# Kernel optimization log

Hardware: AMD Instinct MI355X
Metric: run time of the kernel (lower is better)

The kernel has to match this reference:

```python
import jax, jax.numpy as jnp
import numpy as np

N, E, B, DIM, NF, EF, HID = 16384, 32768, 512, 64, 14, 4, 128

def _p(key, shape, scale):
    return jax.random.normal(key, shape, dtype=jnp.float32) * scale

def setup_inputs() -> dict:
    key = jax.random.key(0)
    ks = jax.random.split(key, 20)
    s = lambda fan: 1.0 / float(np.sqrt(fan))
    z = lambda *sh: jnp.zeros(sh, jnp.float32)
    return {
        "x": jax.random.normal(ks[0], (N, NF), dtype=jnp.float32),
        "edge_index": jax.random.randint(ks[1], (2, E), 0, N),
        "edge_attr": jax.random.uniform(ks[2], (E, EF), dtype=jnp.float32),
        "batch": jnp.sort(jax.random.randint(ks[3], (N,), 0, B)),
        "do_dropout": 0,
        "mlp_drop": 0,
        "lin0_w": _p(ks[4], (NF, DIM), s(NF)), "lin0_b": z(DIM),
        "nn1_w": _p(ks[5], (EF, HID), s(EF)), "nn1_b": z(HID),
        "nn2_w": _p(ks[6], (HID, DIM * DIM), s(HID)), "nn2_b": z(DIM * DIM),
        "root_w": _p(ks[7], (DIM, DIM), s(DIM)), "conv_b": z(DIM),
        "gru_w_ih": _p(ks[8], (3 * DIM, DIM), s(DIM)), "gru_w_hh": _p(ks[9], (3 * DIM, DIM), s(DIM)),
        "gru_b_ih": _p(ks[10], (3 * DIM,), s(DIM)), "gru_b_hh": _p(ks[11], (3 * DIM,), s(DIM)),
        "lstm_w_ih": _p(ks[12], (4 * DIM, 2 * DIM), s(DIM)), "lstm_w_hh": _p(ks[13], (4 * DIM, DIM), s(DIM)),
        "lstm_b_ih": _p(ks[14], (4 * DIM,), s(DIM)), "lstm_b_hh": _p(ks[15], (4 * DIM,), s(DIM)),
        "lin1_w": _p(ks[16], (2 * DIM, DIM), s(2 * DIM)), "lin1_b": z(DIM),
        "lin2_w": _p(ks[17], (DIM, 1), s(DIM)), "lin2_b": z(1),
    }

def _forward(x, edge_attr, lin0_w, lin0_b, nn1_w, nn1_b, nn2_w, nn2_b, root_w, conv_b,
             gru_w_ih, gru_w_hh, gru_b_ih, gru_b_hh,
             lstm_w_ih, lstm_w_hh, lstm_b_ih, lstm_b_hh,
             lin1_w, lin1_b, lin2_w, lin2_b, edge_index, batch):
    src, dst = edge_index[0], edge_index[1]
    out = jax.nn.relu(x @ lin0_w + lin0_b)                      # [N, DIM]
    h = out
    # Edge-conditioned weights (edge_attr is layer-independent -> compute once)
    ew = jax.nn.relu(edge_attr @ nn1_w + nn1_b) @ nn2_w + nn2_b  # [E, DIM*DIM]
    ew = ew.reshape(E, DIM, DIM)
    deg = jax.ops.segment_sum(jnp.ones((E,), jnp.float32), dst, num_segments=N)
    deg = jnp.maximum(deg, 1.0)[:, None]                        # mean aggregation denominator

    def gru_cell(xin, hprev):
        gi = xin @ gru_w_ih.T + gru_b_ih
        gh = hprev @ gru_w_hh.T + gru_b_hh
        ir, iz, inn = jnp.split(gi, 3, axis=-1)
        hr, hz, hn = jnp.split(gh, 3, axis=-1)
        r = jax.nn.sigmoid(ir + hr)
        zg = jax.nn.sigmoid(iz + hz)
        n = jnp.tanh(inn + r * hn)
        return (1.0 - zg) * n + zg * hprev

    for _ in range(3):  # 3 message-passing rounds (structurally fixed)
        msg = jnp.einsum('ed,edf->ef', out[src], ew)            # gather -> per-edge matvec
        agg = jax.ops.segment_sum(msg, dst, num_segments=N) / deg
        m = jax.nn.relu(out @ root_w + agg + conv_b)            # NNConv (root weight + mean aggr)
        h = gru_cell(m, h)
        out = h

    # Set2Set pooling, 3 processing steps
    q_star = jnp.zeros((B, 2 * DIM), jnp.float32)
    hl = jnp.zeros((B, DIM), jnp.float32)
    cl = jnp.zeros((B, DIM), jnp.float32)
    for _ in range(3):
        gates = q_star @ lstm_w_ih.T + lstm_b_ih + hl @ lstm_w_hh.T + lstm_b_hh
        ii, ff, gg, oo = jnp.split(gates, 4, axis=-1)
        cl = jax.nn.sigmoid(ff) * cl + jax.nn.sigmoid(ii) * jnp.tanh(gg)
        hl = jax.nn.sigmoid(oo) * jnp.tanh(cl)
        q = hl                                                  # [B, DIM]
        e = jnp.sum(out * q[batch], axis=-1)                    # [N]
        emax = jax.ops.segment_max(e, batch, num_segments=B)
        ex = jnp.exp(e - emax[batch])
        esum = jnp.maximum(jax.ops.segment_sum(ex, batch, num_segments=B), 1e-16)
        a = ex / esum[batch]                                    # segment softmax
        r = jax.ops.segment_sum(a[:, None] * out, batch, num_segments=B)
        q_star = jnp.concatenate([q, r], axis=-1)               # [B, 2*DIM]

    y = jax.nn.relu(q_star @ lin1_w + lin1_b)
    # dropout flags are False (eval) -> identity
    y = y @ lin2_w + lin2_b
    return y.reshape(-1)                                        # [B]

def reference(x, edge_index, edge_attr, batch, do_dropout, mlp_drop,
              lin0_w, lin0_b, nn1_w, nn1_b, nn2_w, nn2_b, root_w, conv_b,
              gru_w_ih, gru_w_hh, gru_b_ih, gru_b_hh,
              lstm_w_ih, lstm_w_hh, lstm_b_ih, lstm_b_hh,
              lin1_w, lin1_b, lin2_w, lin2_b):
    return _forward(x, edge_attr, lin0_w, lin0_b, nn1_w, nn1_b, nn2_w, nn2_b, root_w, conv_b,
                    gru_w_ih, gru_w_hh, gru_b_ih, gru_b_hh,
                    lstm_w_ih, lstm_w_hh, lstm_b_ih, lstm_b_hh,
                    lin1_w, lin1_b, lin2_w, lin2_b, edge_index, batch)
```

## Files before the change

kernel.cpp:

```cpp
#include <hip/hip_runtime.h>
#include <math.h>

#define N_NODES 16384
#define N_EDGES 32768
#define NGRAPH  512
#define DIM     64
#define NF      14
#define HIDN    128
#define EWCOLS  4096

typedef unsigned short u16;
typedef unsigned int   u32;
typedef __attribute__((ext_vector_type(8))) short bf16x8;
typedef __attribute__((ext_vector_type(4))) float f32x4;
typedef __attribute__((ext_vector_type(4))) u32   u32x4;

__device__ inline float b2f(u16 u){
    unsigned int x = ((unsigned int)u) << 16;
    return __builtin_bit_cast(float, x);
}
__device__ inline u16 f2b(float f){
    unsigned int x = __builtin_bit_cast(unsigned int, f);
    unsigned int r = (x + 0x7FFFu + ((x >> 16) & 1u)) >> 16;
    return (u16)r;
}
__device__ inline float sigf(float x){ return 1.f / (1.f + expf(-x)); }

__global__ __launch_bounds__(256) void k_lin0(const float* __restrict__ x,
        const float* __restrict__ w, const float* __restrict__ b, float* __restrict__ out){
    int n = (blockIdx.x * blockDim.x + threadIdx.x) >> 6;
    int lane = threadIdx.x & 63;
    if (n >= N_NODES) return;
    float xv = (lane < NF) ? x[n * NF + lane] : 0.f;
    float acc = b[lane];
    #pragma unroll
    for (int d = 0; d < NF; ++d){
        float xd = __shfl(xv, d);
        acc += xd * w[d * DIM + lane];
    }
    out[n * DIM + lane] = fmaxf(acc, 0.f);
}

__global__ __launch_bounds__(256) void k_prep(const float* __restrict__ w2,
        const float* __restrict__ lwih, const float* __restrict__ lwhh,
        const float* __restrict__ root, const float* __restrict__ gwih, const float* __restrict__ gwhh,
        u16* __restrict__ w2T, float* __restrict__ wihT, float* __restrict__ whhT,
        u16* __restrict__ rtHi, u16* __restrict__ rtLo,
        u16* __restrict__ wihHi, u16* __restrict__ wihLo,
        u16* __restrict__ whhHi, u16* __restrict__ whhLo){
    int i = blockIdx.x * 256 + threadIdx.x;
    if (i < 524288){
        int k = i >> 12, c = i & 4095;
        w2T[c * HIDN + k] = f2b(w2[i]);
    } else if (i < 557056){
        int i2 = i - 524288;
        int j = i2 >> 7, d = i2 & 127;
        wihT[d * 256 + j] = lwih[i2];
    } else if (i < 573440){
        int i2 = i - 557056;
        int j = i2 >> 6, d = i2 & 63;
        whhT[d * 256 + j] = lwhh[i2];
    } else if (i < 577536){
        int i2 = i - 573440;
        int d = i2 >> 6, j = i2 & 63;
        float v = root[i2]; u16 h = f2b(v);
        rtHi[j * 64 + d] = h; rtLo[j * 64 + d] = f2b(v - b2f(h));
    } else if (i < 589824){
        int k = i - 577536;
        float v = gwih[k]; u16 h = f2b(v);
        wihHi[k] = h; wihLo[k] = f2b(v - b2f(h));
    } else if (i < 602112){
        int k = i - 589824;
        float v = gwhh[k]; u16 h = f2b(v);
        whhHi[k] = h; whhLo[k] = f2b(v - b2f(h));
    }
}

__global__ __launch_bounds__(256) void k_deg(const int* __restrict__ ei, unsigned* __restrict__ degu){
    int e = blockIdx.x * blockDim.x + threadIdx.x;
    if (e < N_EDGES) atomicAdd(&degu[ei[N_EDGES + e]], 1u);
}
__global__ __launch_bounds__(256) void k_dinv(const unsigned* __restrict__ degu, float* __restrict__ dinv){
    int n = blockIdx.x * blockDim.x + threadIdx.x;
    if (n < N_NODES) dinv[n] = 1.f / fmaxf((float)degu[n], 1.f);
}

#define EB   64
#define LDO  68

__global__ __launch_bounds__(256) void k_msg_fused(
        const int* __restrict__ ei, const float* __restrict__ ea,
        const float* __restrict__ w1, const float* __restrict__ b1,
        const u16* __restrict__ w2T, const float* __restrict__ b2,
        const float* __restrict__ out, float* __restrict__ agg)
{
    __shared__ float s_out[EB * LDO];
    __shared__ u16   s_b[2][64 * 128];
    __shared__ float s_w1[512];
    __shared__ float s_b1[128];
    int tid = threadIdx.x;
    int e0 = blockIdx.x * EB;

    s_w1[tid] = w1[tid];
    s_w1[tid + 256] = w1[tid + 256];
    if (tid < 128) s_b1[tid] = b1[tid];
    {
        int row = tid >> 2, cb = (tid & 3) * 16;
        int s = ei[e0 + row];
        const float4* sp = (const float4*)(out + (size_t)s * DIM + cb);
        float4 v0 = sp[0], v1 = sp[1], v2 = sp[2], v3 = sp[3];
        float* dst = s_out + row * LDO + cb;
        *(float4*)(dst)      = v0;
        *(float4*)(dst + 4)  = v1;
        *(float4*)(dst + 8)  = v2;
        *(float4*)(dst + 12) = v3;
    }
    __syncthreads();

    int wv = tid >> 6, lane = tid & 63;
    int WR = (wv >> 1) * 32, WC = (wv & 1) * 32;
    int lr = lane & 15, lk = (lane >> 4) * 8;

    bf16x8 afr[2][4];
    #pragma unroll
    for (int m = 0; m < 2; ++m){
        int erow = e0 + WR + m*16 + lr;
        float4 av = *(const float4*)(ea + (size_t)erow * 4);
        #pragma unroll
        for (int kk = 0; kk < 4; ++kk){
            bf16x8 t8;
            #pragma unroll
            for (int i = 0; i < 8; ++i){
                int h = kk*32 + lk + i;
                float acc = s_b1[h] + av.x*s_w1[h] + av.y*s_w1[128+h]
                          + av.z*s_w1[256+h] + av.w*s_w1[384+h];
                t8[i] = (short)f2b(fmaxf(acc, 0.f));
            }
            afr[m][kk] = t8;
        }
    }

    int bc = tid >> 2, bs = tid & 3;
    const u32x4* gb = (const u32x4*)w2T;
    u32x4 rg[4];
    #pragma unroll
    for (int q = 0; q < 4; ++q) rg[q] = gb[((size_t)bc << 4) + bs*4 + q];

    f32x4 msg[2][2] = {};
    int swzr = (lr & 7) << 4;
    int swzw = (bc & 7) << 4;
    int crow = (lane >> 4) * 4;

    for (int d = 0; d < 64; ++d){
        char* sw = (char*)s_b[d & 1];
        #pragma unroll
        for (int q = 0; q < 4; ++q)
            *(u32x4*)(sw + ((bc*256 + (bs*4+q)*16) ^ swzw)) = rg[q];
        if (d < 63){
            #pragma unroll
            for (int q = 0; q < 4; ++q)
                rg[q] = gb[(((size_t)(d+1)*64 + bc) << 4) + bs*4 + q];
        }
        __syncthreads();
        const char* sr = (const char*)s_b[d & 1];
        f32x4 ew[2][2] = {};
        #pragma unroll
        for (int kk = 0; kk < 4; ++kk){
            int kb = kk*64 + (lane >> 4) * 16;
            bf16x8 bf0 = *(const bf16x8*)(sr + (((WC + lr)*256 + kb)      ^ swzr));
            bf16x8 bf1 = *(const bf16x8*)(sr + (((WC + 16 + lr)*256 + kb) ^ swzr));
            ew[0][0] = __builtin_amdgcn_mfma_f32_16x16x32_bf16(afr[0][kk], bf0, ew[0][0], 0, 0, 0);
            ew[0][1] = __builtin_amdgcn_mfma_f32_16x16x32_bf16(afr[0][kk], bf1, ew[0][1], 0, 0, 0);
            ew[1][0] = __builtin_amdgcn_mfma_f32_16x16x32_bf16(afr[1][kk], bf0, ew[1][0], 0, 0, 0);
            ew[1][1] = __builtin_amdgcn_mfma_f32_16x16x32_bf16(afr[1][kk], bf1, ew[1][1], 0, 0, 0);
        }
        int f0 = d*64 + WC + lr;
        float b2v0 = b2[f0], b2v1 = b2[f0 + 16];
        #pragma unroll
        for (int m = 0; m < 2; ++m){
            #pragma unroll
            for (int r = 0; r < 4; ++r){
                float sc = s_out[(WR + m*16 + crow + r) * LDO + d];
                msg[m][0][r] += sc * (ew[m][0][r] + b2v0);
                msg[m][1][r] += sc * (ew[m][1][r] + b2v1);
            }
        }
    }

    #pragma unroll
    for (int m = 0; m < 2; ++m){
        #pragma unroll
        for (int r = 0; r < 4; ++r){
            int eg = e0 + WR + m*16 + crow + r;
            int dn = ei[N_EDGES + eg];
            atomicAdd(&agg[(size_t)dn * DIM + WC + lr],      msg[m][0][r]);
            atomicAdd(&agg[(size_t)dn * DIM + WC + 16 + lr], msg[m][1][r]);
        }
    }
}

#define LDH 68
__global__ __launch_bounds__(256) void k_update(
        const u16* __restrict__ rtHi, const u16* __restrict__ rtLo,
        const u16* __restrict__ wihHi, const u16* __restrict__ wihLo,
        const u16* __restrict__ whhHi, const u16* __restrict__ whhLo,
        const float* __restrict__ convb, const float* __restrict__ bih,
        const float* __restrict__ bhh,
        const float* __restrict__ agg, const float* __restrict__ dinv,
        float* __restrict__ out)
{
    __shared__ float s_h[64 * LDH];
    __shared__ float s_aux[64 * LDH];
    __shared__ float s_m[64 * LDH];
    int tid = threadIdx.x;
    int n0 = blockIdx.x * 64;

    {
        int row = tid >> 2, cb = (tid & 3) * 16;
        const float4* hp = (const float4*)(out + (size_t)(n0 + row) * DIM + cb);
        const float4* ap = (const float4*)(agg + (size_t)(n0 + row) * DIM + cb);
        float di = dinv[n0 + row];
        #pragma unroll
        for (int q = 0; q < 4; ++q){
            float4 hv = hp[q];
            float4 av = ap[q];
            *(float4*)(s_h + row * LDH + cb + q*4) = hv;
            float4 xv;
            xv.x = av.x * di + convb[cb + q*4 + 0];
            xv.y = av.y * di + convb[cb + q*4 + 1];
            xv.z = av.z * di + convb[cb + q*4 + 2];
            xv.w = av.w * di + convb[cb + q*4 + 3];
            *(float4*)(s_aux + row * LDH + cb + q*4) = xv;
        }
    }
    __syncthreads();

    int wv = tid >> 6, lane = tid & 63;
    int lr = lane & 15, lkb = (lane >> 4) * 8;
    int arow = wv * 16 + lr;

    bf16x8 hHi[2], hLo[2];
    #pragma unroll
    for (int kk = 0; kk < 2; ++kk){
        const float* src = s_h + arow * LDH + kk*32 + lkb;
        bf16x8 hi8, lo8;
        #pragma unroll
        for (int e = 0; e < 8; ++e){
            float v = src[e];
            u16 h = f2b(v);
            hi8[e] = (short)h;
            lo8[e] = (short)f2b(v - b2f(h));
        }
        hHi[kk] = hi8; hLo[kk] = lo8;
    }

    f32x4 c1[4] = {};
    #pragma unroll
    for (int ct = 0; ct < 4; ++ct){
        #pragma unroll
        for (int kk = 0; kk < 2; ++kk){
            int off = (ct*16 + lr) * 64 + kk*32 + lkb;
            bf16x8 bHi = *(const bf16x8*)(rtHi + off);
            bf16x8 bLo = *(const bf16x8*)(rtLo + off);
            c1[ct] = __builtin_amdgcn_mfma_f32_16x16x32_bf16(hHi[kk], bHi, c1[ct], 0, 0, 0);
            c1[ct] = __builtin_amdgcn_mfma_f32_16x16x32_bf16(hLo[kk], bHi, c1[ct], 0, 0, 0);
            c1[ct] = __builtin_amdgcn_mfma_f32_16x16x32_bf16(hHi[kk], bLo, c1[ct], 0, 0, 0);
        }
    }

    int crow = (lane >> 4) * 4;
    #pragma unroll
    for (int ct = 0; ct < 4; ++ct){
        #pragma unroll
        for (int r = 0; r < 4; ++r){
            int row = wv*16 + crow + r;
            int col = ct*16 + lr;
            float m = fmaxf(c1[ct][r] + s_aux[row * LDH + col], 0.f);
            s_m[row * LDH + col] = m;
        }
    }
    __syncthreads();

    bf16x8 mHi[2], mLo[2];
    #pragma unroll
    for (int kk = 0; kk < 2; ++kk){
        const float* src = s_m + arow * LDH + kk*32 + lkb;
        bf16x8 hi8, lo8;
        #pragma unroll
        for (int e = 0; e < 8; ++e){
            float v = src[e];
            u16 h = f2b(v);
            hi8[e] = (short)h;
            lo8[e] = (short)f2b(v - b2f(h));
        }
        mHi[kk] = hi8; mLo[kk] = lo8;
    }

    f32x4 gi[12] = {}, gh[12] = {};
    #pragma unroll
    for (int ct = 0; ct < 12; ++ct){
        #pragma unroll
        for (int kk = 0; kk < 2; ++kk){
            int off = (ct*16 + lr) * 64 + kk*32 + lkb;
            bf16x8 biH = *(const bf16x8*)(wihHi + off);
            bf16x8 biL = *(const bf16x8*)(wihLo + off);
            gi[ct] = __builtin_amdgcn_mfma_f32_16x16x32_bf16(mHi[kk], biH, gi[ct], 0, 0, 0);
            gi[ct] = __builtin_amdgcn_mfma_f32_16x16x32_bf16(mLo[kk], biH, gi[ct], 0, 0, 0);
            gi[ct] = __builtin_amdgcn_mfma_f32_16x16x32_bf16(mHi[kk], biL, gi[ct], 0, 0, 0);
            bf16x8 bhH = *(const bf16x8*)(whhHi + off);
            bf16x8 bhL = *(const bf16x8*)(whhLo + off);
            gh[ct] = __builtin_amdgcn_mfma_f32_16x16x32_bf16(hHi[kk], bhH, gh[ct], 0, 0, 0);
            gh[ct] = __builtin_amdgcn_mfma_f32_16x16x32_bf16(hLo[kk], bhH, gh[ct], 0, 0, 0);
            gh[ct] = __builtin_amdgcn_mfma_f32_16x16x32_bf16(hHi[kk], bhL, gh[ct], 0, 0, 0);
        }
    }

    #pragma unroll
    for (int ct = 0; ct < 4; ++ct){
        int col = ct*16 + lr;
        float br_i = bih[col],       br_h = bhh[col];
        float bz_i = bih[64 + col],  bz_h = bhh[64 + col];
        float bn_i = bih[128 + col], bn_h = bhh[128 + col];
        #pragma unroll
        for (int r = 0; r < 4; ++r){
            int row = wv*16 + crow + r;
            float rg = sigf(gi[ct][r] + br_i + gh[ct][r] + br_h);
            float zg = sigf(gi[ct+4][r] + bz_i + gh[ct+4][r] + bz_h);
            float ng = tanhf(gi[ct+8][r] + bn_i + rg * (gh[ct+8][r] + bn_h));
            float h  = s_h[row * LDH + col];
            s_aux[row * LDH + col] = (1.f - zg) * ng + zg * h;
        }
    }
    __syncthreads();

    {
        int row = tid >> 2, cb = (tid & 3) * 16;
        #pragma unroll
        for (int q = 0; q < 4; ++q)
            *(float4*)(out + (size_t)(n0 + row) * DIM + cb + q*4) =
                *(const float4*)(s_aux + row * LDH + cb + q*4);
    }
}

__global__ __launch_bounds__(256) void k_s2s(
        const float* __restrict__ out, const int* __restrict__ batch,
        const float* __restrict__ wihT, const float* __restrict__ lbih,
        const float* __restrict__ whhT, const float* __restrict__ lbhh,
        const float* __restrict__ l1w, const float* __restrict__ l1b,
        const float* __restrict__ l2w, const float* __restrict__ l2b,
        float* __restrict__ ebuf, float* __restrict__ y)
{
    __shared__ float s_q[128];
    __shared__ float s_hc[128];
    __shared__ float s_g[256];
    __shared__ float s_rw[256];
    __shared__ float s_sw[8];
    __shared__ int   s_rng[2];
    int g = blockIdx.x, tid = threadIdx.x;
    if (tid < 2){
        int target = g + tid;
        int lo = 0, hi = N_NODES;
        while (lo < hi){ int mid = (lo + hi) >> 1; if (batch[mid] < target) lo = mid + 1; else hi = mid; }
        s_rng[tid] = lo;
    }
    if (tid < 128){ s_q[tid] = 0.f; s_hc[tid] = 0.f; }
    __syncthreads();
    int s0 = s_rng[0], s1 = s_rng[1];
    int wv = tid >> 6, lane = tid & 63;

    for (int step = 0; step < 3; ++step){
        float acc = lbih[tid] + lbhh[tid];
        #pragma unroll 8
        for (int d = 0; d < 128; ++d) acc += s_q[d] * wihT[d * 256 + tid];
        #pragma unroll 8
        for (int d = 0; d < 64;  ++d) acc += s_hc[d] * whhT[d * 256 + tid];
        s_g[tid] = acc;
        __syncthreads();
        if (tid < 64){
            float c = sigf(s_g[64 + tid]) * s_hc[64 + tid] + sigf(s_g[tid]) * tanhf(s_g[128 + tid]);
            float h = sigf(s_g[192 + tid]) * tanhf(c);
            s_hc[tid] = h; s_hc[64 + tid] = c;
            s_q[tid] = h;
        }
        __syncthreads();
        float q = s_hc[lane];
        float emx = -3.4e38f;
        for (int n = s0 + wv; n < s1; n += 4){
            float v = out[(size_t)n * DIM + lane] * q;
            #pragma unroll
            for (int off = 32; off; off >>= 1) v += __shfl_xor(v, off);
            if (lane == 0) ebuf[n] = v;
            emx = fmaxf(emx, v);
        }
        if (lane == 0) s_sw[wv] = emx;
        __syncthreads();
        float gmax = fmaxf(fmaxf(s_sw[0], s_sw[1]), fmaxf(s_sw[2], s_sw[3]));
        float rl = 0.f, ss = 0.f;
        for (int n = s0 + wv; n < s1; n += 4){
            float ex = expf(ebuf[n] - gmax);
            rl += ex * out[(size_t)n * DIM + lane];
            ss += ex;
        }
        s_rw[wv * 64 + lane] = rl;
        if (lane == 0) s_sw[4 + wv] = ss;
        __syncthreads();
        if (tid < 64){
            float r = s_rw[tid] + s_rw[64 + tid] + s_rw[128 + tid] + s_rw[192 + tid];
            float S = fmaxf(s_sw[4] + s_sw[5] + s_sw[6] + s_sw[7], 1e-16f);
            s_q[64 + tid] = r / S;
        }
        __syncthreads();
    }
    if (wv == 0){
        float acc = l1b[lane];
        #pragma unroll 8
        for (int d = 0; d < 128; ++d) acc += s_q[d] * l1w[d * 64 + lane];
        float h = fmaxf(acc, 0.f);
        float p = h * l2w[lane];
        #pragma unroll
        for (int off = 32; off; off >>= 1) p += __shfl_down(p, off);
        if (lane == 0) y[g] = p + l2b[0];
    }
}

extern "C" void kernel_launch(void* const* d_in, const int* in_sizes, int n_in,
                              void* d_out, int out_size, void* d_ws, size_t ws_size,
                              hipStream_t stream){
    const float* x      = (const float*)d_in[0];
    const int*   ei     = (const int*)d_in[1];
    const float* ea     = (const float*)d_in[2];
    const int*   batch  = (const int*)d_in[3];
    const float* lin0_w = (const float*)d_in[6];
    const float* lin0_b = (const float*)d_in[7];
    const float* nn1_w  = (const float*)d_in[8];
    const float* nn1_b  = (const float*)d_in[9];
    const float* nn2_w  = (const float*)d_in[10];
    const float* nn2_b  = (const float*)d_in[11];
    const float* root_w = (const float*)d_in[12];
    const float* conv_b = (const float*)d_in[13];
    const float* gwih   = (const float*)d_in[14];
    const float* gwhh   = (const float*)d_in[15];
    const float* gbih   = (const float*)d_in[16];
    const float* gbhh   = (const float*)d_in[17];
    const float* lwih   = (const float*)d_in[18];
    const float* lwhh   = (const float*)d_in[19];
    const float* lbih   = (const float*)d_in[20];
    const float* lbhh   = (const float*)d_in[21];
    const float* l1w    = (const float*)d_in[22];
    const float* l1b    = (const float*)d_in[23];
    const float* l2w    = (const float*)d_in[24];
    const float* l2b    = (const float*)d_in[25];
    float* y = (float*)d_out;

    char* p = (char*)d_ws;
    float* out   = (float*)p;    p += (size_t)N_NODES * DIM * 4;
    float* agg   = (float*)p;    p += (size_t)N_NODES * DIM * 4;
    u16* w2T     = (u16*)p;      p += (size_t)EWCOLS * HIDN * 2;
    float* wihT  = (float*)p;    p += 128 * 256 * 4;
    float* whhT  = (float*)p;    p += 64 * 256 * 4;
    u16* rtHi    = (u16*)p;      p += 4096 * 2;
    u16* rtLo    = (u16*)p;      p += 4096 * 2;
    u16* wihHi   = (u16*)p;      p += 12288 * 2;
    u16* wihLo   = (u16*)p;      p += 12288 * 2;
    u16* whhHi   = (u16*)p;      p += 12288 * 2;
    u16* whhLo   = (u16*)p;      p += 12288 * 2;
    unsigned* degu = (unsigned*)p; p += N_NODES * 4;
    float* dinv  = (float*)p;    p += N_NODES * 4;
    float* ebuf  = (float*)p;    p += N_NODES * 4;

    if ((size_t)(p - (char*)d_ws) > ws_size) return;

    hipMemsetAsync(degu, 0, N_NODES * 4, stream);

    k_prep<<<2352, 256, 0, stream>>>(nn2_w, lwih, lwhh, root_w, gwih, gwhh,
                w2T, wihT, whhT, rtHi, rtLo, wihHi, wihLo, whhHi, whhLo);
    k_lin0<<<N_NODES / 4, 256, 0, stream>>>(x, lin0_w, lin0_b, out);
    k_deg <<<N_EDGES / 256, 256, 0, stream>>>(ei, degu);
    k_dinv<<<N_NODES / 256, 256, 0, stream>>>(degu, dinv);

    for (int r = 0; r < 3; ++r){
        hipMemsetAsync(agg, 0, (size_t)N_NODES * DIM * 4, stream);
        k_msg_fused<<<N_EDGES / EB, 256, 0, stream>>>(ei, ea, nn1_w, nn1_b, w2T, nn2_b, out, agg);
        k_update   <<<N_NODES / 64, 256, 0, stream>>>(rtHi, rtLo, wihHi, wihLo, whhHi, whhLo,
                        conv_b, gbih, gbhh, agg, dinv, out);
    }

    k_s2s<<<NGRAPH, 256, 0, stream>>>(out, batch, wihT, lbih, whhT, lbhh,
                l1w, l1b, l2w, l2b, ebuf, y);
}
```

Before: 370.0 us.

## Double edge tile per message block to halve nn2 weight streaming; stage bias in LDS

```diff
diff --git a/kernel.cpp b/kernel.cpp
--- a/kernel.cpp
+++ b/kernel.cpp
@@ -85,10 +85,10 @@
     if (n < N_NODES) dinv[n] = 1.f / fmaxf((float)degu[n], 1.f);
 }
 
-#define EB   64
+#define EB   128
 #define LDO  68
 
-__global__ __launch_bounds__(256) void k_msg_fused(
+__global__ __launch_bounds__(512) void k_msg_fused(
         const int* __restrict__ ei, const float* __restrict__ ea,
         const float* __restrict__ w1, const float* __restrict__ b1,
         const u16* __restrict__ w2T, const float* __restrict__ b2,
@@ -96,14 +96,19 @@
 {
     __shared__ float s_out[EB * LDO];
     __shared__ u16   s_b[2][64 * 128];
+    __shared__ float s_b2[EWCOLS];
     __shared__ float s_w1[512];
     __shared__ float s_b1[128];
     int tid = threadIdx.x;
     int e0 = blockIdx.x * EB;
 
     s_w1[tid] = w1[tid];
-    s_w1[tid + 256] = w1[tid + 256];
     if (tid < 128) s_b1[tid] = b1[tid];
+    {
+        int base = tid * 8;
+        *(float4*)(s_b2 + base)     = *(const float4*)(b2 + base);
+        *(float4*)(s_b2 + base + 4) = *(const float4*)(b2 + base + 4);
+    }
     {
         int row = tid >> 2, cb = (tid & 3) * 16;
         int s = ei[e0 + row];
@@ -140,11 +145,10 @@
         }
     }
 
-    int bc = tid >> 2, bs = tid & 3;
+    int bc = tid >> 3, bs = tid & 7;
     const u32x4* gb = (const u32x4*)w2T;
-    u32x4 rg[4];
-    #pragma unroll
-    for (int q = 0; q < 4; ++q) rg[q] = gb[((size_t)bc << 4) + bs*4 + q];
+    u32x4 r0 = gb[((size_t)bc << 4) + bs*2];
+    u32x4 r1 = gb[((size_t)bc << 4) + bs*2 + 1];
 
     f32x4 msg[2][2] = {};
     int swzr = (lr & 7) << 4;
@@ -153,13 +157,12 @@
 
     for (int d = 0; d < 64; ++d){
         char* sw = (char*)s_b[d & 1];
-        #pragma unroll
-        for (int q = 0; q < 4; ++q)
-            *(u32x4*)(sw + ((bc*256 + (bs*4+q)*16) ^ swzw)) = rg[q];
+        *(u32x4*)(sw + ((bc*256 + bs*32)      ^ swzw)) = r0;
+        *(u32x4*)(sw + ((bc*256 + bs*32 + 16) ^ swzw)) = r1;
         if (d < 63){
-            #pragma unroll
-            for (int q = 0; q < 4; ++q)
-                rg[q] = gb[(((size_t)(d+1)*64 + bc) << 4) + bs*4 + q];
+            size_t base = ((size_t)(d+1)*64 + bc) << 4;
+            r0 = gb[base + bs*2];
+            r1 = gb[base + bs*2 + 1];
         }
         __syncthreads();
         const char* sr = (const char*)s_b[d & 1];
@@ -174,8 +177,8 @@
             ew[1][0] = __builtin_amdgcn_mfma_f32_16x16x32_bf16(afr[1][kk], bf0, ew[1][0], 0, 0, 0);
             ew[1][1] = __builtin_amdgcn_mfma_f32_16x16x32_bf16(afr[1][kk], bf1, ew[1][1], 0, 0, 0);
         }
-        int f0 = d*64 + WC + lr;
-        float b2v0 = b2[f0], b2v1 = b2[f0 + 16];
+        float b2v0 = s_b2[d*64 + WC + lr];
+        float b2v1 = s_b2[d*64 + WC + 16 + lr];
         #pragma unroll
         for (int m = 0; m < 2; ++m){
             #pragma unroll
@@ -348,7 +351,7 @@
         const float* __restrict__ whhT, const float* __restrict__ lbhh,
         const float* __restrict__ l1w, const float* __restrict__ l1b,
         const float* __restrict__ l2w, const float* __restrict__ l2b,
-        float* __restrict__ ebuf, float* __restrict__ y)
+        float* __restrict__ y)
 {
     __shared__ float s_q[128];
     __shared__ float s_hc[128];
@@ -389,7 +392,6 @@
             float v = out[(size_t)n * DIM + lane] * q;
             #pragma unroll
             for (int off = 32; off; off >>= 1) v += __shfl_xor(v, off);
-            if (lane == 0) ebuf[n] = v;
             emx = fmaxf(emx, v);
         }
         if (lane == 0) s_sw[wv] = emx;
@@ -397,8 +399,12 @@
         float gmax = fmaxf(fmaxf(s_sw[0], s_sw[1]), fmaxf(s_sw[2], s_sw[3]));
         float rl = 0.f, ss = 0.f;
         for (int n = s0 + wv; n < s1; n += 4){
-            float ex = expf(ebuf[n] - gmax);
-            rl += ex * out[(size_t)n * DIM + lane];
+            float o = out[(size_t)n * DIM + lane];
+            float v = o * q;
+            #pragma unroll
+            for (int off = 32; off; off >>= 1) v += __shfl_xor(v, off);
+            float ex = expf(v - gmax);
+            rl += ex * o;
             ss += ex;
         }
         s_rw[wv * 64 + lane] = rl;
@@ -466,7 +472,6 @@
     u16* whhLo   = (u16*)p;      p += 12288 * 2;
     unsigned* degu = (unsigned*)p; p += N_NODES * 4;
     float* dinv  = (float*)p;    p += N_NODES * 4;
-    float* ebuf  = (float*)p;    p += N_NODES * 4;
 
     if ((size_t)(p - (char*)d_ws) > ws_size) return;
 
@@ -480,11 +485,11 @@
 
     for (int r = 0; r < 3; ++r){
         hipMemsetAsync(agg, 0, (size_t)N_NODES * DIM * 4, stream);
-        k_msg_fused<<<N_EDGES / EB, 256, 0, stream>>>(ei, ea, nn1_w, nn1_b, w2T, nn2_b, out, agg);
+        k_msg_fused<<<N_EDGES / EB, 512, 0, stream>>>(ei, ea, nn1_w, nn1_b, w2T, nn2_b, out, agg);
         k_update   <<<N_NODES / 64, 256, 0, stream>>>(rtHi, rtLo, wihHi, wihLo, whhHi, whhLo,
                         conv_b, gbih, gbhh, agg, dinv, out);
     }
 
     k_s2s<<<NGRAPH, 256, 0, stream>>>(out, batch, wihT, lbih, whhT, lbhh,
-                l1w, l1b, l2w, l2b, ebuf, y);
-}
+                l1w, l1b, l2w, l2b, y);
+}
```

Result: faster. 300.9 us (-18.7%).
